# Kernel optimization log

Hardware: AMD Instinct MI355X
Metric: run time of the kernel (lower is better)

The kernel has to match this reference:

```python
import jax, jax.numpy as jnp
import numpy as np
import math

N, DIM = 131072, 128
NUM_CODEBOOKS, CODEBOOK_SIZE = 4, 2048
COMMIT_COST = 0.25


def setup_inputs() -> dict:
    key = jax.random.key(0)
    k1, k2 = jax.random.split(key)
    z_e = jax.random.normal(k1, (N, DIM), dtype=jnp.float32)
    codebooks = jax.random.normal(k2, (NUM_CODEBOOKS, CODEBOOK_SIZE, DIM), dtype=jnp.float32) / math.sqrt(DIM)
    return {"z_e": z_e, "codebooks": codebooks}


def _rvq(z_e, codebooks):
    # Sequential residual quantization stages via scan over codebooks.
    def stage(residual, codebook):
        x_norm = jnp.sum(residual * residual, axis=1, keepdims=True)
        c_norm = jnp.sum(codebook * codebook, axis=1)[None, :]
        d = x_norm - 2.0 * (residual @ codebook.T) + c_norm
        idx = jnp.argmin(d, axis=1)            # [N]
        q = codebook[idx]                      # [N, dim]
        return residual - q, (q, idx)

    _, (qs, idxs) = jax.lax.scan(stage, z_e, codebooks)
    quantized_sum = jnp.sum(qs, axis=0)        # [N, dim]
    codes = idxs.T                             # [N, num_codebooks]
    return quantized_sum, codes


def reference(z_e, codebooks):
    quantized_sum, codes = _rvq(z_e, codebooks)
    sg = jax.lax.stop_gradient
    codebook_loss = jnp.mean((sg(quantized_sum) - z_e) ** 2)
    commit_loss = jnp.mean((quantized_sum - sg(z_e)) ** 2)
    loss = codebook_loss + COMMIT_COST * commit_loss
    # straight-through estimator
    z_q = z_e + sg(quantized_sum - z_e)
    return (z_q, codes, loss)
```

## Files before the change

### kernel.cpp

```cpp
#include <hip/hip_runtime.h>

typedef float v16f __attribute__((ext_vector_type(16)));
typedef _Float16 v8h __attribute__((ext_vector_type(8)));

#define NROWS 131072
#define DIM 128
#define NCB 4
#define CBS 2048
#define ZQ_SIZE ((size_t)NROWS * DIM)
#define CODES_SIZE ((size_t)NROWS * NCB)
#define CHUNK_BYTES 16384
#define CBQ_TOTAL ((size_t)NCB * 64 * CHUNK_BYTES)
#define INV4096 2.44140625e-4f

#define MFMA16(a, b, c) __builtin_amdgcn_mfma_f32_32x32x16_f16((a), (b), (c), 0, 0, 0)

__global__ void prep_cb(const float* __restrict__ cb, _Float16* __restrict__ cbq) {
    const int g = blockIdx.x * 256 + threadIdx.x;
    const int c   = g & 7;
    const int col = (g >> 3) & 31;
    const int q   = (g >> 8) & 63;
    const int s   = g >> 14;
    const float* src = cb + (size_t)(s * CBS + q * 32 + col) * DIM + 16 * c;
    _Float16* base = cbq + (size_t)(s * 64 + q) * 8192;
#pragma unroll
    for (int hh = 0; hh < 2; ++hh) {
        v8h p0, p1;
#pragma unroll
        for (int j = 0; j < 8; ++j) {
            const float v = src[8 * hh + j];
            const _Float16 h0 = (_Float16)v;
            const float t = v - (float)h0;
            p0[j] = h0;
            p1[j] = (_Float16)(t * 4096.0f);
        }
        *reinterpret_cast<v8h*>(base + (size_t)c * 512 + (hh * 32 + col) * 8) = p0;
        *reinterpret_cast<v8h*>(base + (size_t)(8 + c) * 512 + (hh * 32 + col) * 8) = p1;
    }
}

__global__ void prep_cn(const float* __restrict__ cb, float* __restrict__ cn) {
    const int g = blockIdx.x * 256 + threadIdx.x;
    const float* src = cb + (size_t)g * DIM;
    float acc = 0.0f;
    for (int i = 0; i < 32; ++i) {
        const float4 v = *reinterpret_cast<const float4*>(src + 4 * i);
        acc = fmaf(v.x, v.x, acc); acc = fmaf(v.y, v.y, acc);
        acc = fmaf(v.z, v.z, acc); acc = fmaf(v.w, v.w, acc);
    }
    cn[g] = acc;
}

__device__ __forceinline__ void split3(float v, _Float16* h0, _Float16* h1, _Float16* h2) {
    const _Float16 a = (_Float16)v;
    const float t1 = v - (float)a;
    const float s1 = t1 * 4096.0f;
    const _Float16 b = (_Float16)s1;
    const float s2 = (s1 - (float)b) * 4096.0f;
    *h0 = a; *h1 = b; *h2 = (_Float16)s2;
}

__global__ __launch_bounds__(256, 3)
void rvq_main(const float* __restrict__ ze, const float* __restrict__ cbf,
              const _Float16* __restrict__ cbq, const float* __restrict__ cn,
              float* __restrict__ out)
{
    __shared__ __align__(16) char BB[2][CHUNK_BYTES];
    __shared__ int BIs[4][32];

    const int tid  = threadIdx.x;
    const int wid  = tid >> 6;
    const int lane = tid & 63;
    const int col  = lane & 31;
    const int h    = lane >> 5;
    const int rowbase = blockIdx.x * 128 + wid * 32;
    const int myrow   = rowbase + col;

    const float* zrow = ze + (size_t)myrow * DIM + 8 * h;
    _Float16* a2 = (_Float16*)out + (size_t)blockIdx.x * 32768;

    v8h A0[8], A1[8];
    int mylast = 0;

    for (int s = 0; s < NCB; ++s) {
        float pc[8];
        if (s == 0) {
#pragma unroll
            for (int c = 0; c < 8; ++c) {
                const float4 v0 = *reinterpret_cast<const float4*>(zrow + 16 * c);
                const float4 v1 = *reinterpret_cast<const float4*>(zrow + 16 * c + 4);
                float v[8] = {v0.x, v0.y, v0.z, v0.w, v1.x, v1.y, v1.z, v1.w};
                v8h a2v;
                float p[8];
#pragma unroll
                for (int j = 0; j < 8; ++j) {
                    p[j] = v[j] * v[j];
                    _Float16 x0, x1, x2;
                    split3(v[j], &x0, &x1, &x2);
                    A0[c][j] = x0; A1[c][j] = x1; a2v[j] = x2;
                }
                *reinterpret_cast<v8h*>(a2 + ((size_t)c * 256 + tid) * 8) = a2v;
                pc[c] = ((p[0] + p[1]) + (p[2] + p[3])) + ((p[4] + p[5]) + (p[6] + p[7]));
            }
        } else {
            const float* qrow = cbf + ((size_t)((s - 1) * CBS) + mylast) * DIM + 8 * h;
#pragma unroll
            for (int c = 0; c < 8; ++c) {
                const v8h a2v_old = *reinterpret_cast<const v8h*>(a2 + ((size_t)c * 256 + tid) * 8);
                const float4 q0 = *reinterpret_cast<const float4*>(qrow + 16 * c);
                const float4 q1 = *reinterpret_cast<const float4*>(qrow + 16 * c + 4);
                const float qv[8] = {q0.x, q0.y, q0.z, q0.w, q1.x, q1.y, q1.z, q1.w};
                v8h a2v;
                float p[8];
#pragma unroll
                for (int j = 0; j < 8; ++j) {
                    const float vr = fmaf((float)a2v_old[j], 0x1p-24f,
                                     fmaf((float)A1[c][j], 0x1p-12f, (float)A0[c][j]));
                    const float v = vr - qv[j];
                    p[j] = v * v;
                    _Float16 x0, x1, x2;
                    split3(v, &x0, &x1, &x2);
                    A0[c][j] = x0; A1[c][j] = x1; a2v[j] = x2;
                }
                *reinterpret_cast<v8h*>(a2 + ((size_t)c * 256 + tid) * 8) = a2v;
                pc[c] = ((p[0] + p[1]) + (p[2] + p[3])) + ((p[4] + p[5]) + (p[6] + p[7]));
            }
        }
        const float xnp = ((pc[0] + pc[1]) + (pc[2] + pc[3])) + ((pc[4] + pc[5]) + (pc[6] + pc[7]));
        const float xn_own = xnp + __shfl_xor(xnp, 32);
        float xns[16];
#pragma unroll
        for (int r = 0; r < 16; ++r)
            xns[r] = __shfl(xn_own, (r & 3) + 8 * (r >> 2) + 4 * h);

        const char* cbq_s = (const char*)cbq + (size_t)(s * 64) * CHUNK_BYTES;

#pragma unroll
        for (int i = 0; i < 4; ++i) {
            const int blk = i * 4 + wid;
            __builtin_amdgcn_global_load_lds(
                (const __attribute__((address_space(1))) void*)(cbq_s + blk * 1024 + lane * 16),
                (__attribute__((address_space(3))) void*)(&BB[0][blk * 1024]), 16, 0, 0);
        }
        __syncthreads();

        float bestd[16]; int besti[16];
#pragma unroll
        for (int r = 0; r < 16; ++r) { bestd[r] = INFINITY; besti[r] = 0; }

#pragma unroll 1
        for (int q = 0; q < 64; ++q) {
            const int cur = q & 1;
            const float cnv = cn[s * CBS + q * 32 + col];
            if (q < 63) {
                const char* gq = cbq_s + (size_t)(q + 1) * CHUNK_BYTES;
#pragma unroll
                for (int i = 0; i < 4; ++i) {
                    const int blk = i * 4 + wid;
                    __builtin_amdgcn_global_load_lds(
                        (const __attribute__((address_space(1))) void*)(gq + blk * 1024 + lane * 16),
                        (__attribute__((address_space(3))) void*)(&BB[cur ^ 1][blk * 1024]), 16, 0, 0);
                }
            }
            const char* bb = &BB[cur][0];
            v16f aM, aC;
            __builtin_amdgcn_s_setprio(1);
            {
                const v8h b0 = *reinterpret_cast<const v8h*>(bb + lane * 16);
                const v8h b1 = *reinterpret_cast<const v8h*>(bb + 8 * 1024 + lane * 16);
                const v16f Z = {0.f,0.f,0.f,0.f,0.f,0.f,0.f,0.f,0.f,0.f,0.f,0.f,0.f,0.f,0.f,0.f};
                aM = MFMA16(A0[0], b0, Z);
                aC = MFMA16(A1[0], b0, Z);
                aC = MFMA16(A0[0], b1, aC);
            }
#pragma unroll
            for (int c = 1; c < 8; ++c) {
                const v8h b0 = *reinterpret_cast<const v8h*>(bb + (size_t)c * 1024 + lane * 16);
                const v8h b1 = *reinterpret_cast<const v8h*>(bb + (size_t)(8 + c) * 1024 + lane * 16);
                aM = MFMA16(A0[c], b0, aM);
                aC = MFMA16(A1[c], b0, aC);
                aC = MFMA16(A0[c], b1, aC);
            }
            __builtin_amdgcn_s_setprio(0);
            const int code = (q << 5) | col;
#pragma unroll
            for (int r = 0; r < 16; ++r) {
                const float dotf = fmaf(aC[r], INV4096, aM[r]);
                const float d = fmaf(-2.0f, dotf, xns[r]) + cnv;
                const bool take = d < bestd[r];
                bestd[r] = take ? d : bestd[r];
                besti[r] = take ? code : besti[r];
            }
            __syncthreads();
        }

#pragma unroll
        for (int r = 0; r < 16; ++r) {
            float d = bestd[r]; int bi = besti[r];
#pragma unroll
            for (int m = 1; m <= 16; m <<= 1) {
                const float od = __shfl_xor(d, m);
                const int   oi = __shfl_xor(bi, m);
                const bool take = (od < d) || ((od == d) && (oi < bi));
                d  = take ? od : d;
                bi = take ? oi : bi;
            }
            bestd[r] = d; besti[r] = bi;
        }

        if (col == 0) {
#pragma unroll
            for (int r = 0; r < 16; ++r) {
                const int row16 = (r & 3) + 8 * (r >> 2) + 4 * h;
                BIs[wid][row16] = besti[r];
                out[ZQ_SIZE + (size_t)(rowbase + row16) * NCB + s] = (float)besti[r];
            }
        }
        __syncthreads();
        mylast = BIs[wid][col];
    }

    v8h a2r[8];
#pragma unroll
    for (int c = 0; c < 8; ++c)
        a2r[c] = *reinterpret_cast<const v8h*>(a2 + ((size_t)c * 256 + tid) * 8);
    __syncthreads();

    const float* qrow = cbf + ((size_t)(3 * CBS) + mylast) * DIM + 8 * h;
    float lsum = 0.0f;
#pragma unroll
    for (int c = 0; c < 8; ++c) {
        const float4 q0 = *reinterpret_cast<const float4*>(qrow + 16 * c);
        const float4 q1 = *reinterpret_cast<const float4*>(qrow + 16 * c + 4);
        const float4 z0 = *reinterpret_cast<const float4*>(zrow + 16 * c);
        const float4 z1 = *reinterpret_cast<const float4*>(zrow + 16 * c + 4);
        const float qv[8] = {q0.x, q0.y, q0.z, q0.w, q1.x, q1.y, q1.z, q1.w};
        const float zv[8] = {z0.x, z0.y, z0.z, z0.w, z1.x, z1.y, z1.z, z1.w};
        float o[8];
#pragma unroll
        for (int j = 0; j < 8; ++j) {
            const float vr = fmaf((float)a2r[c][j], 0x1p-24f,
                             fmaf((float)A1[c][j], 0x1p-12f, (float)A0[c][j]));
            const float v = vr - qv[j];
            o[j] = zv[j] - v;
            lsum = fmaf(v, v, lsum);
        }
        float4 o0 = {o[0], o[1], o[2], o[3]};
        float4 o1 = {o[4], o[5], o[6], o[7]};
        float* orow = out + (size_t)myrow * DIM + 16 * c + 8 * h;
        *reinterpret_cast<float4*>(orow) = o0;
        *reinterpret_cast<float4*>(orow + 4) = o1;
    }
#pragma unroll
    for (int m = 1; m < 64; m <<= 1) lsum += __shfl_xor(lsum, m);
    if (lane == 0)
        atomicAdd(out + ZQ_SIZE + CODES_SIZE, lsum * (1.25f / 16777216.0f));
}

extern "C" void kernel_launch(void* const* d_in, const int* in_sizes, int n_in,
                              void* d_out, int out_size, void* d_ws, size_t ws_size,
                              hipStream_t stream)
{
    const float* ze  = (const float*)d_in[0];
    const float* cbf = (const float*)d_in[1];
    float* out = (float*)d_out;

    _Float16* cbq = (_Float16*)d_ws;
    float* cnall = (float*)((char*)d_ws + CBQ_TOTAL);

    (void)hipMemsetAsync(out + ZQ_SIZE + CODES_SIZE, 0, sizeof(float), stream);

    prep_cb<<<256, 256, 0, stream>>>(cbf, cbq);
    prep_cn<<<32, 256, 0, stream>>>(cbf, cnall);
    rvq_main<<<NROWS / 128, 256, 0, stream>>>(ze, cbf, cbq, cnall, out);
}
```

Measured before the change: 960.9 us.

## Process two 32-row groups per wave to reuse codebook chunks across more rows

New measurement: 1.633 ms. +70.0%, slower.

```diff
diff --git a/kernel.cpp b/kernel.cpp
--- a/kernel.cpp
+++ b/kernel.cpp
@@ -60,79 +60,29 @@
     *h0 = a; *h1 = b; *h2 = (_Float16)s2;
 }
 
-__global__ __launch_bounds__(256, 3)
+__global__ __launch_bounds__(256, 2)
 void rvq_main(const float* __restrict__ ze, const float* __restrict__ cbf,
               const _Float16* __restrict__ cbq, const float* __restrict__ cn,
               float* __restrict__ out)
 {
     __shared__ __align__(16) char BB[2][CHUNK_BYTES];
-    __shared__ int BIs[4][32];
+    __shared__ __align__(16) float XNs[4][64];
+    __shared__ int BIs[4][64];
 
     const int tid  = threadIdx.x;
     const int wid  = tid >> 6;
     const int lane = tid & 63;
     const int col  = lane & 31;
     const int h    = lane >> 5;
-    const int rowbase = blockIdx.x * 128 + wid * 32;
-    const int myrow   = rowbase + col;
-
-    const float* zrow = ze + (size_t)myrow * DIM + 8 * h;
-    _Float16* a2 = (_Float16*)out + (size_t)blockIdx.x * 32768;
-
-    v8h A0[8], A1[8];
-    int mylast = 0;
-
+    const int rowstart = blockIdx.x * 256 + wid * 64;
+
+    _Float16* a2 = (_Float16*)out + (size_t)blockIdx.x * 65536;
+
+    v8h A0[2][8], A1[2][8];
+    int mylast0 = 0, mylast1 = 0;
+
+#pragma unroll 1
     for (int s = 0; s < NCB; ++s) {
-        float pc[8];
-        if (s == 0) {
-#pragma unroll
-            for (int c = 0; c < 8; ++c) {
-                const float4 v0 = *reinterpret_cast<const float4*>(zrow + 16 * c);
-                const float4 v1 = *reinterpret_cast<const float4*>(zrow + 16 * c + 4);
-                float v[8] = {v0.x, v0.y, v0.z, v0.w, v1.x, v1.y, v1.z, v1.w};
-                v8h a2v;
-                float p[8];
-#pragma unroll
-                for (int j = 0; j < 8; ++j) {
-                    p[j] = v[j] * v[j];
-                    _Float16 x0, x1, x2;
-                    split3(v[j], &x0, &x1, &x2);
-                    A0[c][j] = x0; A1[c][j] = x1; a2v[j] = x2;
-                }
-                *reinterpret_cast<v8h*>(a2 + ((size_t)c * 256 + tid) * 8) = a2v;
-                pc[c] = ((p[0] + p[1]) + (p[2] + p[3])) + ((p[4] + p[5]) + (p[6] + p[7]));
-            }
-        } else {
-            const float* qrow = cbf + ((size_t)((s - 1) * CBS) + mylast) * DIM + 8 * h;
-#pragma unroll
-            for (int c = 0; c < 8; ++c) {
-                const v8h a2v_old = *reinterpret_cast<const v8h*>(a2 + ((size_t)c * 256 + tid) * 8);
-                const float4 q0 = *reinterpret_cast<const float4*>(qrow + 16 * c);
-                const float4 q1 = *reinterpret_cast<const float4*>(qrow + 16 * c + 4);
-                const float qv[8] = {q0.x, q0.y, q0.z, q0.w, q1.x, q1.y, q1.z, q1.w};
-                v8h a2v;
-                float p[8];
-#pragma unroll
-                for (int j = 0; j < 8; ++j) {
-                    const float vr = fmaf((float)a2v_old[j], 0x1p-24f,
-                                     fmaf((float)A1[c][j], 0x1p-12f, (float)A0[c][j]));
-                    const float v = vr - qv[j];
-                    p[j] = v * v;
-                    _Float16 x0, x1, x2;
-                    split3(v, &x0, &x1, &x2);
-                    A0[c][j] = x0; A1[c][j] = x1; a2v[j] = x2;
-                }
-                *reinterpret_cast<v8h*>(a2 + ((size_t)c * 256 + tid) * 8) = a2v;
-                pc[c] = ((p[0] + p[1]) + (p[2] + p[3])) + ((p[4] + p[5]) + (p[6] + p[7]));
-            }
-        }
-        const float xnp = ((pc[0] + pc[1]) + (pc[2] + pc[3])) + ((pc[4] + pc[5]) + (pc[6] + pc[7]));
-        const float xn_own = xnp + __shfl_xor(xnp, 32);
-        float xns[16];
-#pragma unroll
-        for (int r = 0; r < 16; ++r)
-            xns[r] = __shfl(xn_own, (r & 3) + 8 * (r >> 2) + 4 * h);
-
         const char* cbq_s = (const char*)cbq + (size_t)(s * 64) * CHUNK_BYTES;
 
 #pragma unroll
@@ -142,11 +92,57 @@
                 (const __attribute__((address_space(1))) void*)(cbq_s + blk * 1024 + lane * 16),
                 (__attribute__((address_space(3))) void*)(&BB[0][blk * 1024]), 16, 0, 0);
         }
+
+#pragma unroll
+        for (int g = 0; g < 2; ++g) {
+            const int ml = g ? mylast1 : mylast0;
+            const float* zr = ze + (size_t)(rowstart + g * 32 + col) * DIM + 8 * h;
+            const float* qr = cbf + ((size_t)((s - 1) * CBS) + ml) * DIM + 8 * h;
+            float pc[8];
+#pragma unroll
+            for (int c = 0; c < 8; ++c) {
+                v8h a2v;
+                float p[8];
+                if (s == 0) {
+                    const float4 v0 = *reinterpret_cast<const float4*>(zr + 16 * c);
+                    const float4 v1 = *reinterpret_cast<const float4*>(zr + 16 * c + 4);
+                    const float v[8] = {v0.x, v0.y, v0.z, v0.w, v1.x, v1.y, v1.z, v1.w};
+#pragma unroll
+                    for (int j = 0; j < 8; ++j) {
+                        p[j] = v[j] * v[j];
+                        _Float16 x0, x1, x2;
+                        split3(v[j], &x0, &x1, &x2);
+                        A0[g][c][j] = x0; A1[g][c][j] = x1; a2v[j] = x2;
+                    }
+                } else {
+                    const v8h a2o = *reinterpret_cast<const v8h*>(a2 + ((size_t)(g * 8 + c) * 256 + tid) * 8);
+                    const float4 q0 = *reinterpret_cast<const float4*>(qr + 16 * c);
+                    const float4 q1 = *reinterpret_cast<const float4*>(qr + 16 * c + 4);
+                    const float qv[8] = {q0.x, q0.y, q0.z, q0.w, q1.x, q1.y, q1.z, q1.w};
+#pragma unroll
+                    for (int j = 0; j < 8; ++j) {
+                        const float vr = fmaf((float)a2o[j], 0x1p-24f,
+                                         fmaf((float)A1[g][c][j], 0x1p-12f, (float)A0[g][c][j]));
+                        const float v = vr - qv[j];
+                        p[j] = v * v;
+                        _Float16 x0, x1, x2;
+                        split3(v, &x0, &x1, &x2);
+                        A0[g][c][j] = x0; A1[g][c][j] = x1; a2v[j] = x2;
+                    }
+                }
+                *reinterpret_cast<v8h*>(a2 + ((size_t)(g * 8 + c) * 256 + tid) * 8) = a2v;
+                pc[c] = ((p[0] + p[1]) + (p[2] + p[3])) + ((p[4] + p[5]) + (p[6] + p[7]));
+            }
+            const float xnp = ((pc[0] + pc[1]) + (pc[2] + pc[3])) + ((pc[4] + pc[5]) + (pc[6] + pc[7]));
+            const float xn_own = xnp + __shfl_xor(xnp, 32);
+            if (h == 0) XNs[wid][g * 32 + col] = xn_own;
+        }
         __syncthreads();
 
-        float bestd[16]; int besti[16];
-#pragma unroll
-        for (int r = 0; r < 16; ++r) { bestd[r] = INFINITY; besti[r] = 0; }
+        float bestd0[16], bestd1[16];
+        unsigned bq0[4] = {0u, 0u, 0u, 0u}, bq1[4] = {0u, 0u, 0u, 0u};
+#pragma unroll
+        for (int r = 0; r < 16; ++r) { bestd0[r] = INFINITY; bestd1[r] = INFINITY; }
 
 #pragma unroll 1
         for (int q = 0; q < 64; ++q) {
@@ -163,93 +159,129 @@
                 }
             }
             const char* bb = &BB[cur][0];
-            v16f aM, aC;
+            v16f aM0, aC0, aM1, aC1;
             __builtin_amdgcn_s_setprio(1);
             {
                 const v8h b0 = *reinterpret_cast<const v8h*>(bb + lane * 16);
                 const v8h b1 = *reinterpret_cast<const v8h*>(bb + 8 * 1024 + lane * 16);
                 const v16f Z = {0.f,0.f,0.f,0.f,0.f,0.f,0.f,0.f,0.f,0.f,0.f,0.f,0.f,0.f,0.f,0.f};
-                aM = MFMA16(A0[0], b0, Z);
-                aC = MFMA16(A1[0], b0, Z);
-                aC = MFMA16(A0[0], b1, aC);
+                aM0 = MFMA16(A0[0][0], b0, Z);
+                aC0 = MFMA16(A1[0][0], b0, Z);
+                aM1 = MFMA16(A0[1][0], b0, Z);
+                aC1 = MFMA16(A1[1][0], b0, Z);
+                aC0 = MFMA16(A0[0][0], b1, aC0);
+                aC1 = MFMA16(A0[1][0], b1, aC1);
             }
 #pragma unroll
             for (int c = 1; c < 8; ++c) {
                 const v8h b0 = *reinterpret_cast<const v8h*>(bb + (size_t)c * 1024 + lane * 16);
                 const v8h b1 = *reinterpret_cast<const v8h*>(bb + (size_t)(8 + c) * 1024 + lane * 16);
-                aM = MFMA16(A0[c], b0, aM);
-                aC = MFMA16(A1[c], b0, aC);
-                aC = MFMA16(A0[c], b1, aC);
+                aM0 = MFMA16(A0[0][c], b0, aM0);
+                aC0 = MFMA16(A1[0][c], b0, aC0);
+                aM1 = MFMA16(A0[1][c], b0, aM1);
+                aC1 = MFMA16(A1[1][c], b0, aC1);
+                aC0 = MFMA16(A0[0][c], b1, aC0);
+                aC1 = MFMA16(A0[1][c], b1, aC1);
             }
             __builtin_amdgcn_s_setprio(0);
-            const int code = (q << 5) | col;
+
+#pragma unroll
+            for (int p = 0; p < 4; ++p) {
+                const float4 xq = *reinterpret_cast<const float4*>(&XNs[wid][8 * p + 4 * h]);
+#pragma unroll
+                for (int j = 0; j < 4; ++j) {
+                    const int r = 4 * p + j;
+                    const int sh = j * 8;
+                    const float dotf = fmaf(aC0[r], INV4096, aM0[r]);
+                    const float d = fmaf(-2.0f, dotf, xq[j]) + cnv;
+                    const bool take = d < bestd0[r];
+                    bestd0[r] = take ? d : bestd0[r];
+                    const unsigned nb = (bq0[p] & ~(255u << sh)) | ((unsigned)q << sh);
+                    bq0[p] = take ? nb : bq0[p];
+                }
+            }
+#pragma unroll
+            for (int p = 0; p < 4; ++p) {
+                const float4 xq = *reinterpret_cast<const float4*>(&XNs[wid][32 + 8 * p + 4 * h]);
+#pragma unroll
+                for (int j = 0; j < 4; ++j) {
+                    const int r = 4 * p + j;
+                    const int sh = j * 8;
+                    const float dotf = fmaf(aC1[r], INV4096, aM1[r]);
+                    const float d = fmaf(-2.0f, dotf, xq[j]) + cnv;
+                    const bool take = d < bestd1[r];
+                    bestd1[r] = take ? d : bestd1[r];
+                    const unsigned nb = (bq1[p] & ~(255u << sh)) | ((unsigned)q << sh);
+                    bq1[p] = take ? nb : bq1[p];
+                }
+            }
+            __syncthreads();
+        }
+
+#pragma unroll
+        for (int g = 0; g < 2; ++g) {
 #pragma unroll
             for (int r = 0; r < 16; ++r) {
-                const float dotf = fmaf(aC[r], INV4096, aM[r]);
-                const float d = fmaf(-2.0f, dotf, xns[r]) + cnv;
-                const bool take = d < bestd[r];
-                bestd[r] = take ? d : bestd[r];
-                besti[r] = take ? code : besti[r];
-            }
-            __syncthreads();
-        }
-
-#pragma unroll
-        for (int r = 0; r < 16; ++r) {
-            float d = bestd[r]; int bi = besti[r];
-#pragma unroll
-            for (int m = 1; m <= 16; m <<= 1) {
-                const float od = __shfl_xor(d, m);
-                const int   oi = __shfl_xor(bi, m);
-                const bool take = (od < d) || ((od == d) && (oi < bi));
-                d  = take ? od : d;
-                bi = take ? oi : bi;
-            }
-            bestd[r] = d; besti[r] = bi;
-        }
-
-        if (col == 0) {
-#pragma unroll
-            for (int r = 0; r < 16; ++r) {
-                const int row16 = (r & 3) + 8 * (r >> 2) + 4 * h;
-                BIs[wid][row16] = besti[r];
-                out[ZQ_SIZE + (size_t)(rowbase + row16) * NCB + s] = (float)besti[r];
+                float d = g ? bestd1[r] : bestd0[r];
+                const unsigned bw = g ? bq1[r >> 2] : bq0[r >> 2];
+                int bi = (int)((bw >> ((r & 3) * 8)) & 255u) * 32 + col;
+#pragma unroll
+                for (int m = 1; m <= 16; m <<= 1) {
+                    const float od = __shfl_xor(d, m);
+                    const int   oi = __shfl_xor(bi, m);
+                    const bool take = (od < d) || ((od == d) && (oi < bi));
+                    d  = take ? od : d;
+                    bi = take ? oi : bi;
+                }
+                if (col == 0) {
+                    const int row16 = (r & 3) + 8 * (r >> 2) + 4 * h;
+                    BIs[wid][g * 32 + row16] = bi;
+                    out[ZQ_SIZE + (size_t)(rowstart + g * 32 + row16) * NCB + s] = (float)bi;
+                }
             }
         }
         __syncthreads();
-        mylast = BIs[wid][col];
+        mylast0 = BIs[wid][col];
+        mylast1 = BIs[wid][32 + col];
     }
 
-    v8h a2r[8];
-#pragma unroll
-    for (int c = 0; c < 8; ++c)
-        a2r[c] = *reinterpret_cast<const v8h*>(a2 + ((size_t)c * 256 + tid) * 8);
+    v8h a2r[2][8];
+#pragma unroll
+    for (int g = 0; g < 2; ++g)
+#pragma unroll
+        for (int c = 0; c < 8; ++c)
+            a2r[g][c] = *reinterpret_cast<const v8h*>(a2 + ((size_t)(g * 8 + c) * 256 + tid) * 8);
     __syncthreads();
 
-    const float* qrow = cbf + ((size_t)(3 * CBS) + mylast) * DIM + 8 * h;
     float lsum = 0.0f;
 #pragma unroll
-    for (int c = 0; c < 8; ++c) {
-        const float4 q0 = *reinterpret_cast<const float4*>(qrow + 16 * c);
-        const float4 q1 = *reinterpret_cast<const float4*>(qrow + 16 * c + 4);
-        const float4 z0 = *reinterpret_cast<const float4*>(zrow + 16 * c);
-        const float4 z1 = *reinterpret_cast<const float4*>(zrow + 16 * c + 4);
-        const float qv[8] = {q0.x, q0.y, q0.z, q0.w, q1.x, q1.y, q1.z, q1.w};
-        const float zv[8] = {z0.x, z0.y, z0.z, z0.w, z1.x, z1.y, z1.z, z1.w};
-        float o[8];
-#pragma unroll
-        for (int j = 0; j < 8; ++j) {
-            const float vr = fmaf((float)a2r[c][j], 0x1p-24f,
-                             fmaf((float)A1[c][j], 0x1p-12f, (float)A0[c][j]));
-            const float v = vr - qv[j];
-            o[j] = zv[j] - v;
-            lsum = fmaf(v, v, lsum);
-        }
-        float4 o0 = {o[0], o[1], o[2], o[3]};
-        float4 o1 = {o[4], o[5], o[6], o[7]};
-        float* orow = out + (size_t)myrow * DIM + 16 * c + 8 * h;
-        *reinterpret_cast<float4*>(orow) = o0;
-        *reinterpret_cast<float4*>(orow + 4) = o1;
+    for (int g = 0; g < 2; ++g) {
+        const int ml = g ? mylast1 : mylast0;
+        const float* qr = cbf + ((size_t)(3 * CBS) + ml) * DIM + 8 * h;
+        const float* zr = ze + (size_t)(rowstart + g * 32 + col) * DIM + 8 * h;
+        float* orow = out + (size_t)(rowstart + g * 32 + col) * DIM + 8 * h;
+#pragma unroll
+        for (int c = 0; c < 8; ++c) {
+            const float4 q0 = *reinterpret_cast<const float4*>(qr + 16 * c);
+            const float4 q1 = *reinterpret_cast<const float4*>(qr + 16 * c + 4);
+            const float4 z0 = *reinterpret_cast<const float4*>(zr + 16 * c);
+            const float4 z1 = *reinterpret_cast<const float4*>(zr + 16 * c + 4);
+            const float qv[8] = {q0.x, q0.y, q0.z, q0.w, q1.x, q1.y, q1.z, q1.w};
+            const float zv[8] = {z0.x, z0.y, z0.z, z0.w, z1.x, z1.y, z1.z, z1.w};
+            float o[8];
+#pragma unroll
+            for (int j = 0; j < 8; ++j) {
+                const float vr = fmaf((float)a2r[g][c][j], 0x1p-24f,
+                                 fmaf((float)A1[g][c][j], 0x1p-12f, (float)A0[g][c][j]));
+                const float v = vr - qv[j];
+                o[j] = zv[j] - v;
+                lsum = fmaf(v, v, lsum);
+            }
+            const float4 o0 = {o[0], o[1], o[2], o[3]};
+            const float4 o1 = {o[4], o[5], o[6], o[7]};
+            *reinterpret_cast<float4*>(orow + 16 * c) = o0;
+            *reinterpret_cast<float4*>(orow + 16 * c + 4) = o1;
+        }
     }
 #pragma unroll
     for (int m = 1; m < 64; m <<= 1) lsum += __shfl_xor(lsum, m);
@@ -272,5 +304,5 @@
 
     prep_cb<<<256, 256, 0, stream>>>(cbf, cbq);
     prep_cn<<<32, 256, 0, stream>>>(cbf, cnall);
-    rvq_main<<<NROWS / 128, 256, 0, stream>>>(ze, cbf, cbq, cnall, out);
-}
+    rvq_main<<<NROWS / 256, 256, 0, stream>>>(ze, cbf, cbq, cnall, out);
+}
```
